# Optimization experiments

Measured on AMD Instinct MI355X. Metric: run time of the kernel, lower is better.

Reference implementation:

```python
import jax, jax.numpy as jnp
import numpy as np

B, L, R, DV = 4, 4096, 8, 64

def setup_inputs() -> dict:
    key = jax.random.key(0)
    k1, k2, k3, k4 = jax.random.split(key, 4)
    return {
        "v": jax.random.normal(k1, (B, L, DV), dtype=jnp.float32),
        "mask": jax.random.randint(k2, (B, 1, L), 0, 2, dtype=jnp.int32),
        "random_attn_1": jax.random.normal(k3, (B, L, R), dtype=jnp.float32),
        "random_attn_2": jax.random.normal(k4, (B, R, L), dtype=jnp.float32),
        "len_q": L,
    }

def reference(v, mask, random_attn_1, random_attn_2, len_q):
    # rank-8 low-rank synthesis of attention scores: [B, len_q, len_q]
    Bm = mask.shape[0]
    scores = jnp.einsum("blr,brm->blm",
                        random_attn_1[:Bm, :len_q, :],
                        random_attn_2[:Bm, :, :len_q])
    scores = jnp.where(mask == 0, jnp.float32(-1e9), scores)
    attn = jax.nn.softmax(scores, axis=-1)  # dropout omitted (eval mode)
    out = jnp.einsum("blm,bmd->bld", attn, v[:Bm, :len_q, :])
    return out, attn
```

## Files before the change

kernel.cpp:

```cpp
#include <hip/hip_runtime.h>
#include <hip/hip_bf16.h>

#define BB  4
#define LL  4096
#define RR  8
#define DVV 64

typedef __bf16 bf16x8 __attribute__((ext_vector_type(8)));
typedef __bf16 bf16x4 __attribute__((ext_vector_type(4)));
typedef float  f32x4  __attribute__((ext_vector_type(4)));
typedef int    i32x4  __attribute__((ext_vector_type(4)));

__global__ __launch_bounds__(256) void prep_kernel(
    const float* __restrict__ v, __bf16* __restrict__ vF) {
  __shared__ __bf16 tl[64][72];
  const int blk = blockIdx.x;
  const int b   = blk >> 6;
  const int m0  = (blk & 63) << 6;
  const int tid = threadIdx.x;

  const float* vb = v + (((size_t)(b * LL + m0)) << 6);
#pragma unroll
  for (int i = 0; i < 16; ++i) {
    const int idx = (i << 8) + tid;
    tl[idx & 63][idx >> 6] = (__bf16)vb[idx];
  }
  __syncthreads();

  const int wv = tid >> 6, ln = tid & 63;
#pragma unroll
  for (int i = 0; i < 2; ++i) {
    const int u  = wv + (i << 2);
    const int cb = u >> 2, gg = u & 3;
    const int d  = gg * 16 + (ln & 15);
    const int c  = cb * 32 + ((ln >> 4) << 3);
    const size_t unit = ((size_t)(b * 128 + (m0 >> 5) + cb) << 2) + gg;
    *(bf16x8*)(vF + (unit << 9) + (ln << 3)) = *(const bf16x8*)&tl[d][c];
  }
}

__global__ __launch_bounds__(512, 4) void attn_main(
    const float* __restrict__ ra1, const float* __restrict__ ra2,
    const int* __restrict__ mask, const __bf16* __restrict__ vF,
    float* __restrict__ out, float* __restrict__ attn) {
  __shared__ __bf16 pbuf[8 * 8 * 512];
  __shared__ float  red[8][8];

  const int wg   = blockIdx.x;
  const int b    = wg >> 9;
  const int row0 = (wg & 511) << 3;
  const int tid  = threadIdx.x;
  const int wave = tid >> 6;
  const int lane = tid & 63;
  const int W    = wave << 9;

  const float* r2 = ra2 + (size_t)b * (RR * LL) + W + (lane << 2);
  f32x4 rA[RR], rB[RR];
#pragma unroll
  for (int r = 0; r < RR; ++r) {
    rA[r] = *(const f32x4*)(r2 + r * LL);
    rB[r] = *(const f32x4*)(r2 + r * LL + 256);
  }
  const int* mp = mask + (size_t)b * LL + W + (lane << 2);
  const i32x4 mAv = *(const i32x4*)mp;
  const i32x4 mBv = *(const i32x4*)(mp + 256);
  f32x4 mA, mB;
#pragma unroll
  for (int j = 0; j < 4; ++j) {
    mA[j] = mAv[j] ? 1.0f : 0.0f;
    mB[j] = mBv[j] ? 1.0f : 0.0f;
  }

  const float* a_base = ra1 + ((size_t)b * LL + row0) * RR;
  char* const  pw     = (char*)pbuf + (wave << 13);

  float part[8];
#pragma unroll
  for (int i = 0; i < 8; ++i) {
    const float* ap = a_base + i * RR;
    f32x4 sA = {0.f, 0.f, 0.f, 0.f}, sB = {0.f, 0.f, 0.f, 0.f};
#pragma unroll
    for (int r = 0; r < RR; ++r) {
      const float a = ap[r];
#pragma unroll
      for (int j = 0; j < 4; ++j) {
        sA[j] = fmaf(a, rA[r][j], sA[j]);
        sB[j] = fmaf(a, rB[r][j], sB[j]);
      }
    }
    f32x4 eA, eB;
#pragma unroll
    for (int j = 0; j < 4; ++j) {
      eA[j] = __expf(sA[j]) * mA[j];
      eB[j] = __expf(sB[j]) * mB[j];
    }
    part[i] = ((eA[0] + eA[1]) + (eA[2] + eA[3])) +
              ((eB[0] + eB[1]) + (eB[2] + eB[3]));

    bf16x4 pA, pB;
#pragma unroll
    for (int j = 0; j < 4; ++j) { pA[j] = (__bf16)eA[j]; pB[j] = (__bf16)eB[j]; }
    const int swz = (i & 7) << 4;
    *(bf16x4*)(pw + (i << 10) + (((lane << 3)) ^ swz))       = pA;
    *(bf16x4*)(pw + (i << 10) + ((512 + (lane << 3)) ^ swz)) = pB;
  }
#pragma unroll
  for (int s = 1; s < 64; s <<= 1)
#pragma unroll
    for (int i = 0; i < 8; ++i) part[i] += __shfl_xor(part[i], s);
  if (lane == 0) {
#pragma unroll
    for (int i = 0; i < 8; ++i) red[i][wave] = part[i];
  }
  __syncthreads();

  float rinv[8];
#pragma unroll
  for (int i = 0; i < 8; ++i) {
    const f32x4 r0 = *(const f32x4*)&red[i][0];
    const f32x4 r1 = *(const f32x4*)&red[i][4];
    rinv[i] = 1.0f / (((r0[0] + r0[1]) + (r0[2] + r0[3])) +
                      ((r1[0] + r1[1]) + (r1[2] + r1[3])));
  }

  const int lrow = lane & 15, kg = lane >> 4;
  const int lr8  = lrow & 7;
  f32x4 acc[4];
#pragma unroll
  for (int g = 0; g < 4; ++g) acc[g] = (f32x4){0.f, 0.f, 0.f, 0.f};
  const __bf16* vFb = vF + ((size_t)b << 18);
  float* attn_base  = attn + ((size_t)b * LL + row0) * LL + W + (lane << 2);

#pragma unroll
  for (int i = 0; i < 8; ++i) {
#pragma unroll
    for (int h = 0; h < 2; ++h) {
      const int t = 2 * i + h;
      const bf16x8 af = *(const bf16x8*)(
          pw + (lr8 << 10) + (((t << 6) + (kg << 4)) ^ (lr8 << 4)));
      const __bf16* vblk =
          vFb + ((size_t)((wave << 4) + t) << 11) + (lane << 3);
#pragma unroll
      for (int g = 0; g < 4; ++g) {
        const bf16x8 bf = *(const bf16x8*)(vblk + (g << 9));
        acc[g] =
            __builtin_amdgcn_mfma_f32_16x16x32_bf16(af, bf, acc[g], 0, 0, 0);
      }
    }
    const int swz = (i & 7) << 4;
    const bf16x4 pA =
        *(const bf16x4*)(pw + (i << 10) + (((lane << 3)) ^ swz));
    const bf16x4 pB =
        *(const bf16x4*)(pw + (i << 10) + ((512 + (lane << 3)) ^ swz));
    f32x4 oA, oB;
#pragma unroll
    for (int j = 0; j < 4; ++j) {
      oA[j] = (float)pA[j] * rinv[i];
      oB[j] = (float)pB[j] * rinv[i];
    }
    *(f32x4*)(attn_base + (size_t)i * LL)       = oA;
    *(f32x4*)(attn_base + (size_t)i * LL + 256) = oB;
  }

  asm volatile("s_waitcnt lgkmcnt(0)\n\ts_barrier" ::: "memory");
  float* osum = (float*)pbuf;
  if (kg < 2) {
#pragma unroll
    for (int g = 0; g < 4; ++g)
#pragma unroll
      for (int ii = 0; ii < 4; ++ii)
        osum[(wave * 8 + kg * 4 + ii) * 64 + g * 16 + lrow] = acc[g][ii];
  }
  asm volatile("s_waitcnt lgkmcnt(0)\n\ts_barrier" ::: "memory");

  if (tid < 128) {
    const int orow = tid >> 4;
    const int d    = (tid & 15) << 2;
    f32x4 o = {0.f, 0.f, 0.f, 0.f};
#pragma unroll
    for (int w = 0; w < 8; ++w) {
      const f32x4 rr = *(const f32x4*)(osum + ((w * 8 + orow) << 6) + d);
#pragma unroll
      for (int j = 0; j < 4; ++j) o[j] += rr[j];
    }
    float rt = 0.f;
#pragma unroll
    for (int w = 0; w < 8; ++w) rt += red[orow][w];
    const float rinv_o = 1.0f / rt;
#pragma unroll
    for (int j = 0; j < 4; ++j) o[j] *= rinv_o;
    *(f32x4*)(out + ((size_t)b * LL + row0 + orow) * DVV + d) = o;
  }
}

extern "C" void kernel_launch(void* const* d_in, const int* in_sizes, int n_in,
                              void* d_out, int out_size, void* d_ws,
                              size_t ws_size, hipStream_t stream) {
  (void)in_sizes; (void)n_in; (void)out_size; (void)ws_size;
  const float* v    = (const float*)d_in[0];
  const int*   mask = (const int*)d_in[1];
  const float* ra1  = (const float*)d_in[2];
  const float* ra2  = (const float*)d_in[3];

  float* out  = (float*)d_out;
  float* attn = out + (size_t)BB * LL * DVV;

  __bf16* vF = (__bf16*)d_ws;

  hipLaunchKernelGGL(prep_kernel, dim3(BB * (LL / 64)), dim3(256), 0, stream,
                     v, vF);
  hipLaunchKernelGGL(attn_main, dim3(BB * LL / 8), dim3(512), 0, stream,
                     ra1, ra2, mask, vF, out, attn);
}
```

Baseline: 317.6 us.

## Process four row blocks per workgroup and defer attn stores into next block

Each workgroup now loops over four 8-row blocks, so the ra2 and mask register loads are reused across blocks and the grid shrinks to 512 workgroups. The normalized attn stores for the previous block are issued inside the next block's score computation, overlapping global writes with exp/FMA work. The cross-wave output reduction now uses a half-size shared buffer with two-phase accumulation. In exchange there are fewer resident workgroups per CU, extra barriers per block, and a possible race on the shared row-sum array between iterations.

```diff
diff --git a/kernel.cpp b/kernel.cpp
--- a/kernel.cpp
+++ b/kernel.cpp
@@ -10,6 +10,9 @@
 typedef __bf16 bf16x4 __attribute__((ext_vector_type(4)));
 typedef float  f32x4  __attribute__((ext_vector_type(4)));
 typedef int    i32x4  __attribute__((ext_vector_type(4)));
+
+#define LGKM_BARRIER() \
+  asm volatile("s_waitcnt lgkmcnt(0)\n\ts_barrier" ::: "memory")
 
 __global__ __launch_bounds__(256) void prep_kernel(
     const float* __restrict__ v, __bf16* __restrict__ vF) {
@@ -44,15 +47,18 @@
     const int* __restrict__ mask, const __bf16* __restrict__ vF,
     float* __restrict__ out, float* __restrict__ attn) {
   __shared__ __bf16 pbuf[8 * 8 * 512];
+  __shared__ float  osum4[4 * 8 * 64];
   __shared__ float  red[8][8];
 
   const int wg   = blockIdx.x;
-  const int b    = wg >> 9;
-  const int row0 = (wg & 511) << 3;
+  const int b    = wg >> 7;
+  const int blk0 = (wg & 127) << 2;
   const int tid  = threadIdx.x;
   const int wave = tid >> 6;
   const int lane = tid & 63;
   const int W    = wave << 9;
+  const int lrow = lane & 15, kg = lane >> 4;
+  const int lr8  = lrow & 7;
 
   const float* r2 = ra2 + (size_t)b * (RR * LL) + W + (lane << 2);
   f32x4 rA[RR], rB[RR];
@@ -71,125 +77,161 @@
     mB[j] = mBv[j] ? 1.0f : 0.0f;
   }
 
-  const float* a_base = ra1 + ((size_t)b * LL + row0) * RR;
-  char* const  pw     = (char*)pbuf + (wave << 13);
-
-  float part[8];
-#pragma unroll
-  for (int i = 0; i < 8; ++i) {
-    const float* ap = a_base + i * RR;
-    f32x4 sA = {0.f, 0.f, 0.f, 0.f}, sB = {0.f, 0.f, 0.f, 0.f};
-#pragma unroll
-    for (int r = 0; r < RR; ++r) {
-      const float a = ap[r];
+  char* const   pw  = (char*)pbuf + (wave << 13);
+  const __bf16* vFb = vF + ((size_t)b << 18);
+
+  float  rinv[8];
+  float* attn_prev = nullptr;
+
+#pragma unroll 1
+  for (int jj = 0; jj < 4; ++jj) {
+    const int row0 = (blk0 + jj) << 3;
+    const float* a_base  = ra1 + ((size_t)b * LL + row0) * RR;
+    float* attn_cur = attn + ((size_t)b * LL + row0) * LL + W + (lane << 2);
+    const bool have_prev = (jj > 0);
+
+    float part[8];
+#pragma unroll
+    for (int i = 0; i < 8; ++i) {
+      const int swz  = i << 4;
+      char* pposA = pw + (i << 10) + (((lane << 3)) ^ swz);
+      char* pposB = pw + (i << 10) + ((512 + (lane << 3)) ^ swz);
+
+      if (have_prev) {
+        const bf16x4 qA = *(const bf16x4*)pposA;
+        const bf16x4 qB = *(const bf16x4*)pposB;
+        f32x4 oA, oB;
+#pragma unroll
+        for (int j = 0; j < 4; ++j) {
+          oA[j] = (float)qA[j] * rinv[i];
+          oB[j] = (float)qB[j] * rinv[i];
+        }
+        *(f32x4*)(attn_prev + (size_t)i * LL)       = oA;
+        *(f32x4*)(attn_prev + (size_t)i * LL + 256) = oB;
+        __builtin_amdgcn_sched_barrier(0);
+      }
+
+      const float* ap = a_base + i * RR;
+      f32x4 sA = {0.f, 0.f, 0.f, 0.f}, sB = {0.f, 0.f, 0.f, 0.f};
+#pragma unroll
+      for (int r = 0; r < RR; ++r) {
+        const float a = ap[r];
+#pragma unroll
+        for (int j = 0; j < 4; ++j) {
+          sA[j] = fmaf(a, rA[r][j], sA[j]);
+          sB[j] = fmaf(a, rB[r][j], sB[j]);
+        }
+      }
+      f32x4 eA, eB;
 #pragma unroll
       for (int j = 0; j < 4; ++j) {
-        sA[j] = fmaf(a, rA[r][j], sA[j]);
-        sB[j] = fmaf(a, rB[r][j], sB[j]);
-      }
-    }
-    f32x4 eA, eB;
-#pragma unroll
-    for (int j = 0; j < 4; ++j) {
-      eA[j] = __expf(sA[j]) * mA[j];
-      eB[j] = __expf(sB[j]) * mB[j];
-    }
-    part[i] = ((eA[0] + eA[1]) + (eA[2] + eA[3])) +
-              ((eB[0] + eB[1]) + (eB[2] + eB[3]));
-
-    bf16x4 pA, pB;
-#pragma unroll
-    for (int j = 0; j < 4; ++j) { pA[j] = (__bf16)eA[j]; pB[j] = (__bf16)eB[j]; }
-    const int swz = (i & 7) << 4;
-    *(bf16x4*)(pw + (i << 10) + (((lane << 3)) ^ swz))       = pA;
-    *(bf16x4*)(pw + (i << 10) + ((512 + (lane << 3)) ^ swz)) = pB;
-  }
-#pragma unroll
-  for (int s = 1; s < 64; s <<= 1)
-#pragma unroll
-    for (int i = 0; i < 8; ++i) part[i] += __shfl_xor(part[i], s);
-  if (lane == 0) {
-#pragma unroll
-    for (int i = 0; i < 8; ++i) red[i][wave] = part[i];
-  }
-  __syncthreads();
-
-  float rinv[8];
-#pragma unroll
-  for (int i = 0; i < 8; ++i) {
-    const f32x4 r0 = *(const f32x4*)&red[i][0];
-    const f32x4 r1 = *(const f32x4*)&red[i][4];
-    rinv[i] = 1.0f / (((r0[0] + r0[1]) + (r0[2] + r0[3])) +
-                      ((r1[0] + r1[1]) + (r1[2] + r1[3])));
-  }
-
-  const int lrow = lane & 15, kg = lane >> 4;
-  const int lr8  = lrow & 7;
-  f32x4 acc[4];
-#pragma unroll
-  for (int g = 0; g < 4; ++g) acc[g] = (f32x4){0.f, 0.f, 0.f, 0.f};
-  const __bf16* vFb = vF + ((size_t)b << 18);
-  float* attn_base  = attn + ((size_t)b * LL + row0) * LL + W + (lane << 2);
-
-#pragma unroll
-  for (int i = 0; i < 8; ++i) {
-#pragma unroll
-    for (int h = 0; h < 2; ++h) {
-      const int t = 2 * i + h;
-      const bf16x8 af = *(const bf16x8*)(
-          pw + (lr8 << 10) + (((t << 6) + (kg << 4)) ^ (lr8 << 4)));
-      const __bf16* vblk =
-          vFb + ((size_t)((wave << 4) + t) << 11) + (lane << 3);
-#pragma unroll
-      for (int g = 0; g < 4; ++g) {
-        const bf16x8 bf = *(const bf16x8*)(vblk + (g << 9));
-        acc[g] =
-            __builtin_amdgcn_mfma_f32_16x16x32_bf16(af, bf, acc[g], 0, 0, 0);
-      }
-    }
-    const int swz = (i & 7) << 4;
-    const bf16x4 pA =
-        *(const bf16x4*)(pw + (i << 10) + (((lane << 3)) ^ swz));
-    const bf16x4 pB =
-        *(const bf16x4*)(pw + (i << 10) + ((512 + (lane << 3)) ^ swz));
-    f32x4 oA, oB;
-#pragma unroll
-    for (int j = 0; j < 4; ++j) {
-      oA[j] = (float)pA[j] * rinv[i];
-      oB[j] = (float)pB[j] * rinv[i];
-    }
-    *(f32x4*)(attn_base + (size_t)i * LL)       = oA;
-    *(f32x4*)(attn_base + (size_t)i * LL + 256) = oB;
-  }
-
-  asm volatile("s_waitcnt lgkmcnt(0)\n\ts_barrier" ::: "memory");
-  float* osum = (float*)pbuf;
-  if (kg < 2) {
-#pragma unroll
-    for (int g = 0; g < 4; ++g)
-#pragma unroll
-      for (int ii = 0; ii < 4; ++ii)
-        osum[(wave * 8 + kg * 4 + ii) * 64 + g * 16 + lrow] = acc[g][ii];
-  }
-  asm volatile("s_waitcnt lgkmcnt(0)\n\ts_barrier" ::: "memory");
-
-  if (tid < 128) {
-    const int orow = tid >> 4;
-    const int d    = (tid & 15) << 2;
-    f32x4 o = {0.f, 0.f, 0.f, 0.f};
-#pragma unroll
-    for (int w = 0; w < 8; ++w) {
-      const f32x4 rr = *(const f32x4*)(osum + ((w * 8 + orow) << 6) + d);
-#pragma unroll
-      for (int j = 0; j < 4; ++j) o[j] += rr[j];
-    }
-    float rt = 0.f;
-#pragma unroll
-    for (int w = 0; w < 8; ++w) rt += red[orow][w];
-    const float rinv_o = 1.0f / rt;
-#pragma unroll
-    for (int j = 0; j < 4; ++j) o[j] *= rinv_o;
-    *(f32x4*)(out + ((size_t)b * LL + row0 + orow) * DVV + d) = o;
+        eA[j] = __expf(sA[j]) * mA[j];
+        eB[j] = __expf(sB[j]) * mB[j];
+      }
+      part[i] = ((eA[0] + eA[1]) + (eA[2] + eA[3])) +
+                ((eB[0] + eB[1]) + (eB[2] + eB[3]));
+
+      bf16x4 pA, pB;
+#pragma unroll
+      for (int j = 0; j < 4; ++j) { pA[j] = (__bf16)eA[j]; pB[j] = (__bf16)eB[j]; }
+      *(bf16x4*)pposA = pA;
+      *(bf16x4*)pposB = pB;
+    }
+
+#pragma unroll
+    for (int s = 1; s < 64; s <<= 1)
+#pragma unroll
+      for (int i = 0; i < 8; ++i) part[i] += __shfl_xor(part[i], s);
+    if (lane == 0) {
+#pragma unroll
+      for (int i = 0; i < 8; ++i) red[i][wave] = part[i];
+    }
+    LGKM_BARRIER();
+
+#pragma unroll
+    for (int i = 0; i < 8; ++i) {
+      const f32x4 r0 = *(const f32x4*)&red[i][0];
+      const f32x4 r1 = *(const f32x4*)&red[i][4];
+      rinv[i] = 1.0f / (((r0[0] + r0[1]) + (r0[2] + r0[3])) +
+                        ((r1[0] + r1[1]) + (r1[2] + r1[3])));
+    }
+
+    f32x4 acc[4];
+#pragma unroll
+    for (int g = 0; g < 4; ++g) acc[g] = (f32x4){0.f, 0.f, 0.f, 0.f};
+#pragma unroll
+    for (int i = 0; i < 8; ++i) {
+#pragma unroll
+      for (int h = 0; h < 2; ++h) {
+        const int t = 2 * i + h;
+        const bf16x8 af = *(const bf16x8*)(
+            pw + (lr8 << 10) + (((t << 6) + (kg << 4)) ^ (lr8 << 4)));
+        const __bf16* vblk =
+            vFb + ((size_t)((wave << 4) + t) << 11) + (lane << 3);
+#pragma unroll
+        for (int g = 0; g < 4; ++g) {
+          const bf16x8 bf = *(const bf16x8*)(vblk + (g << 9));
+          acc[g] =
+              __builtin_amdgcn_mfma_f32_16x16x32_bf16(af, bf, acc[g], 0, 0, 0);
+        }
+      }
+      if (jj == 3) {
+        const int swz = i << 4;
+        const bf16x4 qA =
+            *(const bf16x4*)(pw + (i << 10) + (((lane << 3)) ^ swz));
+        const bf16x4 qB =
+            *(const bf16x4*)(pw + (i << 10) + ((512 + (lane << 3)) ^ swz));
+        f32x4 oA, oB;
+#pragma unroll
+        for (int j = 0; j < 4; ++j) {
+          oA[j] = (float)qA[j] * rinv[i];
+          oB[j] = (float)qB[j] * rinv[i];
+        }
+        *(f32x4*)(attn_cur + (size_t)i * LL)       = oA;
+        *(f32x4*)(attn_cur + (size_t)i * LL + 256) = oB;
+      }
+    }
+
+    LGKM_BARRIER();
+    if (wave >= 4 && kg < 2) {
+#pragma unroll
+      for (int g = 0; g < 4; ++g)
+#pragma unroll
+        for (int ii = 0; ii < 4; ++ii)
+          osum4[((wave - 4) * 8 + kg * 4 + ii) * 64 + g * 16 + lrow] =
+              acc[g][ii];
+    }
+    LGKM_BARRIER();
+    if (wave < 4 && kg < 2) {
+#pragma unroll
+      for (int g = 0; g < 4; ++g)
+#pragma unroll
+        for (int ii = 0; ii < 4; ++ii) {
+          float* p = &osum4[(wave * 8 + kg * 4 + ii) * 64 + g * 16 + lrow];
+          *p += acc[g][ii];
+        }
+    }
+    LGKM_BARRIER();
+    if (tid < 128) {
+      const int orow = tid >> 4;
+      const int d    = (tid & 15) << 2;
+      f32x4 o = {0.f, 0.f, 0.f, 0.f};
+#pragma unroll
+      for (int w = 0; w < 4; ++w) {
+        const f32x4 rr = *(const f32x4*)(osum4 + ((w * 8 + orow) << 6) + d);
+#pragma unroll
+        for (int j = 0; j < 4; ++j) o[j] += rr[j];
+      }
+      float rt = 0.f;
+#pragma unroll
+      for (int w = 0; w < 8; ++w) rt += red[orow][w];
+      const float rinv_o = 1.0f / rt;
+#pragma unroll
+      for (int j = 0; j < 4; ++j) o[j] *= rinv_o;
+      *(f32x4*)(out + ((size_t)b * LL + row0 + orow) * DVV + d) = o;
+    }
+
+    attn_prev = attn_cur;
   }
 }
 
@@ -209,6 +251,6 @@
 
   hipLaunchKernelGGL(prep_kernel, dim3(BB * (LL / 64)), dim3(256), 0, stream,
                      v, vF);
-  hipLaunchKernelGGL(attn_main, dim3(BB * LL / 8), dim3(512), 0, stream,
+  hipLaunchKernelGGL(attn_main, dim3(512), dim3(512), 0, stream,
                      ra1, ra2, mask, vF, out, attn);
 }
```

Measured after the change: 653.8 us. 2.06x slower.
